# Performance work log

Measured on AMD Instinct MI355X. Metric: run time of the kernel, lower is better.

Reference implementation:

```python
import jax, jax.numpy as jnp
import numpy as np

LN_EPS = 1e-5

def setup_inputs() -> dict:
    key = jax.random.key(0)
    k1, k2, k3, k4 = jax.random.split(key, 4)
    B, N, D, E = 2, 50000, 128, 800000
    H = jax.random.normal(k1, (B, N, D), dtype=jnp.float32)
    src = jax.random.randint(k2, (E,), 0, N, dtype=jnp.int64)
    dst = jax.random.randint(k3, (E,), 0, N, dtype=jnp.int64)
    W = jax.random.normal(k4, (D, D), dtype=jnp.float32) * (1.0 / np.sqrt(D))
    gamma = jnp.ones((D,), dtype=jnp.float32)
    beta = jnp.zeros((D,), dtype=jnp.float32)
    return {"H": H, "src": src, "dst": dst, "W": W, "gamma": gamma, "beta": beta}

def reference(H, src, dst, W, gamma, beta):
    # m = Linear(H) (no bias): [B,N,D]
    m = jnp.einsum('bnd,de->bne', H, W)
    # gather messages at src, scatter-add into dst along node dim
    agg = jnp.zeros_like(m).at[:, dst, :].add(m[:, src, :])
    x = H + jax.nn.gelu(agg, approximate=False)
    # LayerNorm over last dim
    mu = jnp.mean(x, axis=-1, keepdims=True)
    var = jnp.var(x, axis=-1, keepdims=True)
    return (x - mu) * jax.lax.rsqrt(var + LN_EPS) * gamma + beta
```

## Files before the change

kernel.cpp:

```cpp
#include <hip/hip_runtime.h>
#include <math.h>

#define DIM 128
#define LN_EPS 1e-5f
#define CAP 64
#define TPW 2

typedef unsigned short bf16_t;
typedef unsigned short u16;
typedef __attribute__((ext_vector_type(8))) short bf16x8;
typedef __attribute__((ext_vector_type(4))) float f32x4;
typedef __attribute__((ext_vector_type(2))) float f32x2;

__device__ __forceinline__ bf16_t f2bf(float f) {
    unsigned u = __builtin_bit_cast(unsigned, f);
    u += 0x7FFFu + ((u >> 16) & 1u);
    return (bf16_t)(u >> 16);
}
__device__ __forceinline__ float lo_bf(unsigned u) {
    return __builtin_bit_cast(float, u << 16);
}
__device__ __forceinline__ float hi_bf(unsigned u) {
    return __builtin_bit_cast(float, u & 0xFFFF0000u);
}

__global__ __launch_bounds__(256) void prep_kernel(
    const float* __restrict__ W, bf16_t* __restrict__ WT,
    int* __restrict__ cursor, int N)
{
    const int tid = blockIdx.x * 256 + threadIdx.x;
    if (tid < N) cursor[tid] = 0;
    if (tid < (DIM * DIM / 4)) {
        const float4 w = ((const float4*)W)[tid];
        const int k  = tid >> 5;
        const int n0 = (tid & 31) * 4;
        WT[(n0 + 0) * DIM + k] = f2bf(w.x);
        WT[(n0 + 1) * DIM + k] = f2bf(w.y);
        WT[(n0 + 2) * DIM + k] = f2bf(w.z);
        WT[(n0 + 3) * DIM + k] = f2bf(w.w);
    }
}

__global__ __launch_bounds__(256, 2) void gemm_fill_kernel(
    const float* __restrict__ Hmat, const bf16_t* __restrict__ WT,
    bf16_t* __restrict__ Mout,
    const int* __restrict__ src, const int* __restrict__ dst,
    int* __restrict__ cursor, u16* __restrict__ eidxT,
    int nrows, int N, int E, int FB)
{
    if ((int)blockIdx.x < FB) {
        const int base = (blockIdx.x * 256 + threadIdx.x) * 8;
        if (base + 7 < E) {
            int4 da = *(const int4*)&dst[base];
            int4 db = *(const int4*)&dst[base + 4];
            int4 sa = *(const int4*)&src[base];
            int4 sb = *(const int4*)&src[base + 4];
            int p0 = atomicAdd(&cursor[da.x], 1);
            int p1 = atomicAdd(&cursor[da.y], 1);
            int p2 = atomicAdd(&cursor[da.z], 1);
            int p3 = atomicAdd(&cursor[da.w], 1);
            int p4 = atomicAdd(&cursor[db.x], 1);
            int p5 = atomicAdd(&cursor[db.y], 1);
            int p6 = atomicAdd(&cursor[db.z], 1);
            int p7 = atomicAdd(&cursor[db.w], 1);
            if (p0 < CAP) eidxT[(size_t)p0 * N + da.x] = (u16)sa.x;
            if (p1 < CAP) eidxT[(size_t)p1 * N + da.y] = (u16)sa.y;
            if (p2 < CAP) eidxT[(size_t)p2 * N + da.z] = (u16)sa.z;
            if (p3 < CAP) eidxT[(size_t)p3 * N + da.w] = (u16)sa.w;
            if (p4 < CAP) eidxT[(size_t)p4 * N + db.x] = (u16)sb.x;
            if (p5 < CAP) eidxT[(size_t)p5 * N + db.y] = (u16)sb.y;
            if (p6 < CAP) eidxT[(size_t)p6 * N + db.z] = (u16)sb.z;
            if (p7 < CAP) eidxT[(size_t)p7 * N + db.w] = (u16)sb.w;
        } else {
            for (int e = base; e < E; ++e) {
                int d = dst[e];
                int pos = atomicAdd(&cursor[d], 1);
                if (pos < CAP) eidxT[(size_t)pos * N + d] = (u16)src[e];
            }
        }
        return;
    }

    const int tid  = threadIdx.x;
    const int wave = tid >> 6;
    const int lane = tid & 63;
    const int quad = lane >> 4;
    const int l15  = lane & 15;

    bf16x8 wf[32];
    #pragma unroll
    for (int t = 0; t < 8; ++t)
        #pragma unroll
        for (int ks = 0; ks < 4; ++ks)
            wf[t * 4 + ks] = *(const bf16x8*)
                &WT[(size_t)(t * 16 + l15) * DIM + ks * 32 + quad * 8];

    const int gblock  = blockIdx.x - FB;
    const int baserow = (gblock * 4 + wave) * (TPW * 16);

    #pragma unroll
    for (int rt = 0; rt < TPW; ++rt) {
        const int arow = baserow + rt * 16 + l15;
        const float* Arow = Hmat + (size_t)((arow < nrows) ? arow : 0) * DIM;

        f32x4 acc[8];
        #pragma unroll
        for (int t = 0; t < 8; ++t) acc[t] = (f32x4){0.f, 0.f, 0.f, 0.f};

        #pragma unroll
        for (int ks = 0; ks < 4; ++ks) {
            const int k0 = ks * 32 + quad * 8;
            float4 a0 = *(const float4*)&Arow[k0];
            float4 a1 = *(const float4*)&Arow[k0 + 4];
            bf16x8 hf;
            hf[0] = (short)f2bf(a0.x); hf[1] = (short)f2bf(a0.y);
            hf[2] = (short)f2bf(a0.z); hf[3] = (short)f2bf(a0.w);
            hf[4] = (short)f2bf(a1.x); hf[5] = (short)f2bf(a1.y);
            hf[6] = (short)f2bf(a1.z); hf[7] = (short)f2bf(a1.w);

            #pragma unroll
            for (int t = 0; t < 8; ++t)
                acc[t] = __builtin_amdgcn_mfma_f32_16x16x32_bf16(
                             wf[t * 4 + ks], hf, acc[t], 0, 0, 0);
        }

        if (arow < nrows) {
            const int b = (arow >= N) ? 1 : 0;
            const int n = arow - (b ? N : 0);
            bf16_t* orow = Mout + ((size_t)n * 2 + b) * DIM;
            #pragma unroll
            for (int t = 0; t < 8; ++t) {
                ushort4 o;
                o.x = f2bf(acc[t][0]); o.y = f2bf(acc[t][1]);
                o.z = f2bf(acc[t][2]); o.w = f2bf(acc[t][3]);
                *(ushort4*)&orow[t * 16 + quad * 4] = o;
            }
        }
    }
}

__global__ __launch_bounds__(256) void gather_kernel(
    const bf16_t* __restrict__ M, const float* __restrict__ Hmat,
    const int* __restrict__ cursor, const u16* __restrict__ eidxT,
    const float* __restrict__ gamma, const float* __restrict__ beta,
    float* __restrict__ out, int N)
{
    const int wave = threadIdx.x >> 6;
    const int lane = threadIdx.x & 63;
    const int node = blockIdx.x * 4 + wave;
    if (node >= N) return;

    const int b  = lane >> 5;
    const int c4 = lane & 31;

    const size_t elembase = ((size_t)b * N + node) * DIM + c4 * 4;
    float4 h  = *(const float4*)&Hmat[elembase];
    float4 gm = *(const float4*)&gamma[c4 * 4];
    float4 bt = *(const float4*)&beta[c4 * 4];

    int cnt = cursor[node];
    if (cnt > CAP) cnt = CAP;

    int myidx = (lane < cnt) ? (int)eidxT[(size_t)lane * N + node] : 0;

    const uint2* M2 = (const uint2*)M;

    f32x2 accA = {0.f, 0.f}, accB = {0.f, 0.f};
    int j = 0;
    for (; j + 16 <= cnt; j += 16) {
        uint2 v[16];
        #pragma unroll
        for (int q = 0; q < 16; ++q) {
            int s = __builtin_amdgcn_readlane(myidx, j + q);
            v[q] = (M2 + ((size_t)s << 6))[lane];
        }
        #pragma unroll
        for (int q = 0; q < 16; ++q) {
            f32x2 p0 = { lo_bf(v[q].x), hi_bf(v[q].x) };
            f32x2 p1 = { lo_bf(v[q].y), hi_bf(v[q].y) };
            accA += p0;
            accB += p1;
        }
    }
    if (j < cnt) {
        uint2 v[16];
        #pragma unroll
        for (int q = 0; q < 16; ++q) {
            int s = __builtin_amdgcn_readlane(myidx, (j + q) & 63);
            v[q] = (M2 + ((size_t)s << 6))[lane];
        }
        #pragma unroll
        for (int q = 0; q < 16; ++q) {
            unsigned vx = (j + q < cnt) ? v[q].x : 0u;
            unsigned vy = (j + q < cnt) ? v[q].y : 0u;
            f32x2 p0 = { lo_bf(vx), hi_bf(vx) };
            f32x2 p1 = { lo_bf(vy), hi_bf(vy) };
            accA += p0;
            accB += p1;
        }
    }

    float acc0 = accA.x, acc1 = accA.y, acc2 = accB.x, acc3 = accB.y;

    const float inv_sqrt2 = 0.70710678118654752f;
    float x0 = h.x + 0.5f * acc0 * (1.f + erff(acc0 * inv_sqrt2));
    float x1 = h.y + 0.5f * acc1 * (1.f + erff(acc1 * inv_sqrt2));
    float x2 = h.z + 0.5f * acc2 * (1.f + erff(acc2 * inv_sqrt2));
    float x3 = h.w + 0.5f * acc3 * (1.f + erff(acc3 * inv_sqrt2));

    float s  = x0 + x1 + x2 + x3;
    float ss = x0 * x0 + x1 * x1 + x2 * x2 + x3 * x3;
    #pragma unroll
    for (int o = 16; o > 0; o >>= 1) {
        s  += __shfl_xor(s,  o, 64);
        ss += __shfl_xor(ss, o, 64);
    }
    const float mean = s * (1.f / DIM);
    const float var  = ss * (1.f / DIM) - mean * mean;
    const float inv  = rsqrtf(var + LN_EPS);

    float4 o;
    o.x = (x0 - mean) * inv * gm.x + bt.x;
    o.y = (x1 - mean) * inv * gm.y + bt.y;
    o.z = (x2 - mean) * inv * gm.z + bt.z;
    o.w = (x3 - mean) * inv * gm.w + bt.w;
    *(float4*)&out[elembase] = o;
}

extern "C" void kernel_launch(void* const* d_in, const int* in_sizes, int n_in,
                              void* d_out, int out_size, void* d_ws, size_t ws_size,
                              hipStream_t stream)
{
    const float* H     = (const float*)d_in[0];
    const int*   src   = (const int*)  d_in[1];
    const int*   dst   = (const int*)  d_in[2];
    const float* W     = (const float*)d_in[3];
    const float* gamma = (const float*)d_in[4];
    const float* beta  = (const float*)d_in[5];
    float* out = (float*)d_out;

    const int E     = in_sizes[1];
    const int total = in_sizes[0];
    const int nrows = total / DIM;
    const int N     = nrows / 2;

    char* ws = (char*)d_ws;
    bf16_t* Mbuf = (bf16_t*)ws;   ws += (size_t)total * sizeof(bf16_t);
    int* cursor  = (int*)ws;      ws += (size_t)N * sizeof(int);
    u16* eidxT   = (u16*)ws;      ws += (size_t)CAP * N * sizeof(u16);
    bf16_t* WT   = (bf16_t*)ws;   ws += (size_t)DIM * DIM * sizeof(bf16_t);

    const int prep_elems = (N > DIM * DIM / 4) ? N : DIM * DIM / 4;
    prep_kernel<<<(prep_elems + 255) / 256, 256, 0, stream>>>(W, WT, cursor, N);

    const int FB = (E + 2047) / 2048;
    const int ROWS_PER_BLOCK = 4 * TPW * 16;
    const int GB = (nrows + ROWS_PER_BLOCK - 1) / ROWS_PER_BLOCK;
    gemm_fill_kernel<<<FB + GB, 256, 0, stream>>>(H, WT, Mbuf, src, dst,
                                                  cursor, eidxT, nrows, N, E, FB);

    gather_kernel<<<(N + 3) / 4, 256, 0, stream>>>(Mbuf, H, cursor, eidxT,
                                                   gamma, beta, out, N);
}
```

Measured before the change: 226.5 us.

## Fuse prep, GEMM/fill and gather into one cooperative persistent kernel

Replaces the three kernel launches with a single cooperative persistent kernel that uses grid-wide syncs between the prep, GEMM-plus-edge-bucketing, and gather/LayerNorm phases. The block count comes from the occupancy query, and 3/8 of the blocks do the edge fill while the rest do the GEMM. The edge index layout changes from transposed [slot][node] to node-major [node][slot], and the gather unrolls 32 loads with per-element predicates. The aim is to remove launch gaps and tail effects. In exchange, grid.sync costs and the fixed split may leave the fill or GEMM side underused, and persistent grid-stride loops may lose some memory parallelism.

New measurement: 569.8 us. +151.5%, slower.

```diff
diff --git a/kernel.cpp b/kernel.cpp
--- a/kernel.cpp
+++ b/kernel.cpp
@@ -1,10 +1,13 @@
 #include <hip/hip_runtime.h>
+#include <hip/hip_cooperative_groups.h>
 #include <math.h>
+
+namespace cg = cooperative_groups;
 
 #define DIM 128
 #define LN_EPS 1e-5f
 #define CAP 64
-#define TPW 2
+#define NTHR 256
 
 typedef unsigned short bf16_t;
 typedef unsigned short u16;
@@ -24,207 +27,183 @@
     return __builtin_bit_cast(float, u & 0xFFFF0000u);
 }
 
-__global__ __launch_bounds__(256) void prep_kernel(
-    const float* __restrict__ W, bf16_t* __restrict__ WT,
-    int* __restrict__ cursor, int N)
+__global__ __launch_bounds__(256, 2) void coop_kernel(
+    const float* __restrict__ Hmat, const int* __restrict__ src,
+    const int* __restrict__ dst, const float* __restrict__ W,
+    const float* __restrict__ gamma, const float* __restrict__ beta,
+    float* __restrict__ out, bf16_t* __restrict__ Mout,
+    int* __restrict__ cursor, u16* __restrict__ eidx,
+    bf16_t* __restrict__ WTg, int N, int nrows, int E)
 {
-    const int tid = blockIdx.x * 256 + threadIdx.x;
-    if (tid < N) cursor[tid] = 0;
-    if (tid < (DIM * DIM / 4)) {
-        const float4 w = ((const float4*)W)[tid];
-        const int k  = tid >> 5;
-        const int n0 = (tid & 31) * 4;
-        WT[(n0 + 0) * DIM + k] = f2bf(w.x);
-        WT[(n0 + 1) * DIM + k] = f2bf(w.y);
-        WT[(n0 + 2) * DIM + k] = f2bf(w.z);
-        WT[(n0 + 3) * DIM + k] = f2bf(w.w);
+    cg::grid_group grid = cg::this_grid();
+    const int tid   = threadIdx.x;
+    const int nblk  = gridDim.x;
+    const int gtid  = blockIdx.x * NTHR + tid;
+    const int lane  = tid & 63;
+    const int wave  = tid >> 6;
+    const int quad  = lane >> 4;
+    const int l15   = lane & 15;
+
+    for (int i = gtid; i < N; i += nblk * NTHR) cursor[i] = 0;
+    if (gtid < DIM * DIM / 4) {
+        const float4 w = ((const float4*)W)[gtid];
+        const int k  = gtid >> 5;
+        const int n0 = (gtid & 31) * 4;
+        WTg[(n0 + 0) * DIM + k] = f2bf(w.x);
+        WTg[(n0 + 1) * DIM + k] = f2bf(w.y);
+        WTg[(n0 + 2) * DIM + k] = f2bf(w.z);
+        WTg[(n0 + 3) * DIM + k] = f2bf(w.w);
     }
-}
-
-__global__ __launch_bounds__(256, 2) void gemm_fill_kernel(
-    const float* __restrict__ Hmat, const bf16_t* __restrict__ WT,
-    bf16_t* __restrict__ Mout,
-    const int* __restrict__ src, const int* __restrict__ dst,
-    int* __restrict__ cursor, u16* __restrict__ eidxT,
-    int nrows, int N, int E, int FB)
-{
-    if ((int)blockIdx.x < FB) {
-        const int base = (blockIdx.x * 256 + threadIdx.x) * 8;
-        if (base + 7 < E) {
-            int4 da = *(const int4*)&dst[base];
-            int4 db = *(const int4*)&dst[base + 4];
-            int4 sa = *(const int4*)&src[base];
-            int4 sb = *(const int4*)&src[base + 4];
-            int p0 = atomicAdd(&cursor[da.x], 1);
-            int p1 = atomicAdd(&cursor[da.y], 1);
-            int p2 = atomicAdd(&cursor[da.z], 1);
-            int p3 = atomicAdd(&cursor[da.w], 1);
-            int p4 = atomicAdd(&cursor[db.x], 1);
-            int p5 = atomicAdd(&cursor[db.y], 1);
-            int p6 = atomicAdd(&cursor[db.z], 1);
-            int p7 = atomicAdd(&cursor[db.w], 1);
-            if (p0 < CAP) eidxT[(size_t)p0 * N + da.x] = (u16)sa.x;
-            if (p1 < CAP) eidxT[(size_t)p1 * N + da.y] = (u16)sa.y;
-            if (p2 < CAP) eidxT[(size_t)p2 * N + da.z] = (u16)sa.z;
-            if (p3 < CAP) eidxT[(size_t)p3 * N + da.w] = (u16)sa.w;
-            if (p4 < CAP) eidxT[(size_t)p4 * N + db.x] = (u16)sb.x;
-            if (p5 < CAP) eidxT[(size_t)p5 * N + db.y] = (u16)sb.y;
-            if (p6 < CAP) eidxT[(size_t)p6 * N + db.z] = (u16)sb.z;
-            if (p7 < CAP) eidxT[(size_t)p7 * N + db.w] = (u16)sb.w;
-        } else {
-            for (int e = base; e < E; ++e) {
-                int d = dst[e];
-                int pos = atomicAdd(&cursor[d], 1);
-                if (pos < CAP) eidxT[(size_t)pos * N + d] = (u16)src[e];
-            }
-        }
-        return;
+    __threadfence();
+    grid.sync();
+
+    const int FBLK = (nblk * 3) / 8;
+    if ((int)blockIdx.x < FBLK) {
+        const int nt = FBLK * NTHR;
+        for (int base = (blockIdx.x * NTHR + tid) * 8; base < E; base += nt * 8) {
+            if (base + 7 < E) {
+                int4 da = *(const int4*)&dst[base];
+                int4 db = *(const int4*)&dst[base + 4];
+                int4 sa = *(const int4*)&src[base];
+                int4 sb = *(const int4*)&src[base + 4];
+                int p0 = atomicAdd(&cursor[da.x], 1);
+                int p1 = atomicAdd(&cursor[da.y], 1);
+                int p2 = atomicAdd(&cursor[da.z], 1);
+                int p3 = atomicAdd(&cursor[da.w], 1);
+                int p4 = atomicAdd(&cursor[db.x], 1);
+                int p5 = atomicAdd(&cursor[db.y], 1);
+                int p6 = atomicAdd(&cursor[db.z], 1);
+                int p7 = atomicAdd(&cursor[db.w], 1);
+                if (p0 < CAP) eidx[(size_t)da.x * CAP + p0] = (u16)sa.x;
+                if (p1 < CAP) eidx[(size_t)da.y * CAP + p1] = (u16)sa.y;
+                if (p2 < CAP) eidx[(size_t)da.z * CAP + p2] = (u16)sa.z;
+                if (p3 < CAP) eidx[(size_t)da.w * CAP + p3] = (u16)sa.w;
+                if (p4 < CAP) eidx[(size_t)db.x * CAP + p4] = (u16)sb.x;
+                if (p5 < CAP) eidx[(size_t)db.y * CAP + p5] = (u16)sb.y;
+                if (p6 < CAP) eidx[(size_t)db.z * CAP + p6] = (u16)sb.z;
+                if (p7 < CAP) eidx[(size_t)db.w * CAP + p7] = (u16)sb.w;
+            } else {
+                for (int e = base; e < E; ++e) {
+                    int d = dst[e];
+                    int pos = atomicAdd(&cursor[d], 1);
+                    if (pos < CAP) eidx[(size_t)d * CAP + pos] = (u16)src[e];
+                }
+            }
+        }
+    } else {
+        bf16x8 wf[32];
+        #pragma unroll
+        for (int t = 0; t < 8; ++t)
+            #pragma unroll
+            for (int ks = 0; ks < 4; ++ks)
+                wf[t * 4 + ks] = *(const bf16x8*)
+                    &WTg[(size_t)(t * 16 + l15) * DIM + ks * 32 + quad * 8];
+
+        const int ntiles = (nrows + 15) / 16;
+        const int gw     = (nblk - FBLK) * 4;
+        for (int tile = (blockIdx.x - FBLK) * 4 + wave; tile < ntiles; tile += gw) {
+            const int arow = tile * 16 + l15;
+            const float* Arow = Hmat + (size_t)((arow < nrows) ? arow : 0) * DIM;
+
+            f32x4 acc[8];
+            #pragma unroll
+            for (int t = 0; t < 8; ++t) acc[t] = (f32x4){0.f, 0.f, 0.f, 0.f};
+
+            #pragma unroll
+            for (int ks = 0; ks < 4; ++ks) {
+                const int k0 = ks * 32 + quad * 8;
+                float4 a0 = *(const float4*)&Arow[k0];
+                float4 a1 = *(const float4*)&Arow[k0 + 4];
+                bf16x8 hf;
+                hf[0] = (short)f2bf(a0.x); hf[1] = (short)f2bf(a0.y);
+                hf[2] = (short)f2bf(a0.z); hf[3] = (short)f2bf(a0.w);
+                hf[4] = (short)f2bf(a1.x); hf[5] = (short)f2bf(a1.y);
+                hf[6] = (short)f2bf(a1.z); hf[7] = (short)f2bf(a1.w);
+
+                #pragma unroll
+                for (int t = 0; t < 8; ++t)
+                    acc[t] = __builtin_amdgcn_mfma_f32_16x16x32_bf16(
+                                 wf[t * 4 + ks], hf, acc[t], 0, 0, 0);
+            }
+
+            if (arow < nrows) {
+                const int b = (arow >= N) ? 1 : 0;
+                const int n = arow - (b ? N : 0);
+                bf16_t* orow = Mout + ((size_t)n * 2 + b) * DIM;
+                #pragma unroll
+                for (int t = 0; t < 8; ++t) {
+                    ushort4 o;
+                    o.x = f2bf(acc[t][0]); o.y = f2bf(acc[t][1]);
+                    o.z = f2bf(acc[t][2]); o.w = f2bf(acc[t][3]);
+                    *(ushort4*)&orow[t * 16 + quad * 4] = o;
+                }
+            }
+        }
     }
-
-    const int tid  = threadIdx.x;
-    const int wave = tid >> 6;
-    const int lane = tid & 63;
-    const int quad = lane >> 4;
-    const int l15  = lane & 15;
-
-    bf16x8 wf[32];
-    #pragma unroll
-    for (int t = 0; t < 8; ++t)
-        #pragma unroll
-        for (int ks = 0; ks < 4; ++ks)
-            wf[t * 4 + ks] = *(const bf16x8*)
-                &WT[(size_t)(t * 16 + l15) * DIM + ks * 32 + quad * 8];
-
-    const int gblock  = blockIdx.x - FB;
-    const int baserow = (gblock * 4 + wave) * (TPW * 16);
-
-    #pragma unroll
-    for (int rt = 0; rt < TPW; ++rt) {
-        const int arow = baserow + rt * 16 + l15;
-        const float* Arow = Hmat + (size_t)((arow < nrows) ? arow : 0) * DIM;
-
-        f32x4 acc[8];
-        #pragma unroll
-        for (int t = 0; t < 8; ++t) acc[t] = (f32x4){0.f, 0.f, 0.f, 0.f};
-
-        #pragma unroll
-        for (int ks = 0; ks < 4; ++ks) {
-            const int k0 = ks * 32 + quad * 8;
-            float4 a0 = *(const float4*)&Arow[k0];
-            float4 a1 = *(const float4*)&Arow[k0 + 4];
-            bf16x8 hf;
-            hf[0] = (short)f2bf(a0.x); hf[1] = (short)f2bf(a0.y);
-            hf[2] = (short)f2bf(a0.z); hf[3] = (short)f2bf(a0.w);
-            hf[4] = (short)f2bf(a1.x); hf[5] = (short)f2bf(a1.y);
-            hf[6] = (short)f2bf(a1.z); hf[7] = (short)f2bf(a1.w);
-
-            #pragma unroll
-            for (int t = 0; t < 8; ++t)
-                acc[t] = __builtin_amdgcn_mfma_f32_16x16x32_bf16(
-                             wf[t * 4 + ks], hf, acc[t], 0, 0, 0);
-        }
-
-        if (arow < nrows) {
-            const int b = (arow >= N) ? 1 : 0;
-            const int n = arow - (b ? N : 0);
-            bf16_t* orow = Mout + ((size_t)n * 2 + b) * DIM;
-            #pragma unroll
-            for (int t = 0; t < 8; ++t) {
-                ushort4 o;
-                o.x = f2bf(acc[t][0]); o.y = f2bf(acc[t][1]);
-                o.z = f2bf(acc[t][2]); o.w = f2bf(acc[t][3]);
-                *(ushort4*)&orow[t * 16 + quad * 4] = o;
-            }
-        }
-    }
-}
-
-__global__ __launch_bounds__(256) void gather_kernel(
-    const bf16_t* __restrict__ M, const float* __restrict__ Hmat,
-    const int* __restrict__ cursor, const u16* __restrict__ eidxT,
-    const float* __restrict__ gamma, const float* __restrict__ beta,
-    float* __restrict__ out, int N)
-{
-    const int wave = threadIdx.x >> 6;
-    const int lane = threadIdx.x & 63;
-    const int node = blockIdx.x * 4 + wave;
-    if (node >= N) return;
+    __threadfence();
+    grid.sync();
 
     const int b  = lane >> 5;
     const int c4 = lane & 31;
-
-    const size_t elembase = ((size_t)b * N + node) * DIM + c4 * 4;
-    float4 h  = *(const float4*)&Hmat[elembase];
+    const int nwaves = nblk * 4;
+    const uint2* M2  = (const uint2*)Mout;
+
     float4 gm = *(const float4*)&gamma[c4 * 4];
     float4 bt = *(const float4*)&beta[c4 * 4];
 
-    int cnt = cursor[node];
-    if (cnt > CAP) cnt = CAP;
-
-    int myidx = (lane < cnt) ? (int)eidxT[(size_t)lane * N + node] : 0;
-
-    const uint2* M2 = (const uint2*)M;
-
-    f32x2 accA = {0.f, 0.f}, accB = {0.f, 0.f};
-    int j = 0;
-    for (; j + 16 <= cnt; j += 16) {
-        uint2 v[16];
+    for (int node = blockIdx.x * 4 + wave; node < N; node += nwaves) {
+        int cnt = cursor[node];
+        if (cnt > CAP) cnt = CAP;
+
+        int myidx = (lane < cnt) ? (int)eidx[(size_t)node * CAP + lane] : 0;
+
+        const size_t elembase = ((size_t)b * N + node) * DIM + c4 * 4;
+        float4 h = *(const float4*)&Hmat[elembase];
+
+        f32x2 accA = {0.f, 0.f}, accB = {0.f, 0.f};
+        for (int j = 0; j < cnt; j += 32) {
+            uint2 v[32];
+            #pragma unroll
+            for (int q = 0; q < 32; ++q) {
+                if (j + q < cnt) {
+                    int s = __builtin_amdgcn_readlane(myidx, j + q);
+                    v[q] = (M2 + ((size_t)s << 6))[lane];
+                }
+            }
+            #pragma unroll
+            for (int q = 0; q < 32; ++q) {
+                if (j + q < cnt) {
+                    accA += (f32x2){ lo_bf(v[q].x), hi_bf(v[q].x) };
+                    accB += (f32x2){ lo_bf(v[q].y), hi_bf(v[q].y) };
+                }
+            }
+        }
+        float acc0 = accA.x, acc1 = accA.y, acc2 = accB.x, acc3 = accB.y;
+
+        const float inv_sqrt2 = 0.70710678118654752f;
+        float x0 = h.x + 0.5f * acc0 * (1.f + erff(acc0 * inv_sqrt2));
+        float x1 = h.y + 0.5f * acc1 * (1.f + erff(acc1 * inv_sqrt2));
+        float x2 = h.z + 0.5f * acc2 * (1.f + erff(acc2 * inv_sqrt2));
+        float x3 = h.w + 0.5f * acc3 * (1.f + erff(acc3 * inv_sqrt2));
+
+        float s  = x0 + x1 + x2 + x3;
+        float ss = x0 * x0 + x1 * x1 + x2 * x2 + x3 * x3;
         #pragma unroll
-        for (int q = 0; q < 16; ++q) {
-            int s = __builtin_amdgcn_readlane(myidx, j + q);
-            v[q] = (M2 + ((size_t)s << 6))[lane];
-        }
-        #pragma unroll
-        for (int q = 0; q < 16; ++q) {
-            f32x2 p0 = { lo_bf(v[q].x), hi_bf(v[q].x) };
-            f32x2 p1 = { lo_bf(v[q].y), hi_bf(v[q].y) };
-            accA += p0;
-            accB += p1;
-        }
+        for (int o = 16; o > 0; o >>= 1) {
+            s  += __shfl_xor(s,  o, 64);
+            ss += __shfl_xor(ss, o, 64);
+        }
+        const float mean = s * (1.f / DIM);
+        const float var  = ss * (1.f / DIM) - mean * mean;
+        const float inv  = rsqrtf(var + LN_EPS);
+
+        float4 o;
+        o.x = (x0 - mean) * inv * gm.x + bt.x;
+        o.y = (x1 - mean) * inv * gm.y + bt.y;
+        o.z = (x2 - mean) * inv * gm.z + bt.z;
+        o.w = (x3 - mean) * inv * gm.w + bt.w;
+        *(float4*)&out[elembase] = o;
     }
-    if (j < cnt) {
-        uint2 v[16];
-        #pragma unroll
-        for (int q = 0; q < 16; ++q) {
-            int s = __builtin_amdgcn_readlane(myidx, (j + q) & 63);
-            v[q] = (M2 + ((size_t)s << 6))[lane];
-        }
-        #pragma unroll
-        for (int q = 0; q < 16; ++q) {
-            unsigned vx = (j + q < cnt) ? v[q].x : 0u;
-            unsigned vy = (j + q < cnt) ? v[q].y : 0u;
-            f32x2 p0 = { lo_bf(vx), hi_bf(vx) };
-            f32x2 p1 = { lo_bf(vy), hi_bf(vy) };
-            accA += p0;
-            accB += p1;
-        }
-    }
-
-    float acc0 = accA.x, acc1 = accA.y, acc2 = accB.x, acc3 = accB.y;
-
-    const float inv_sqrt2 = 0.70710678118654752f;
-    float x0 = h.x + 0.5f * acc0 * (1.f + erff(acc0 * inv_sqrt2));
-    float x1 = h.y + 0.5f * acc1 * (1.f + erff(acc1 * inv_sqrt2));
-    float x2 = h.z + 0.5f * acc2 * (1.f + erff(acc2 * inv_sqrt2));
-    float x3 = h.w + 0.5f * acc3 * (1.f + erff(acc3 * inv_sqrt2));
-
-    float s  = x0 + x1 + x2 + x3;
-    float ss = x0 * x0 + x1 * x1 + x2 * x2 + x3 * x3;
-    #pragma unroll
-    for (int o = 16; o > 0; o >>= 1) {
-        s  += __shfl_xor(s,  o, 64);
-        ss += __shfl_xor(ss, o, 64);
-    }
-    const float mean = s * (1.f / DIM);
-    const float var  = ss * (1.f / DIM) - mean * mean;
-    const float inv  = rsqrtf(var + LN_EPS);
-
-    float4 o;
-    o.x = (x0 - mean) * inv * gm.x + bt.x;
-    o.y = (x1 - mean) * inv * gm.y + bt.y;
-    o.z = (x2 - mean) * inv * gm.z + bt.z;
-    o.w = (x3 - mean) * inv * gm.w + bt.w;
-    *(float4*)&out[elembase] = o;
 }
 
 extern "C" void kernel_launch(void* const* d_in, const int* in_sizes, int n_in,
@@ -239,26 +218,30 @@
     const float* beta  = (const float*)d_in[5];
     float* out = (float*)d_out;
 
-    const int E     = in_sizes[1];
-    const int total = in_sizes[0];
-    const int nrows = total / DIM;
-    const int N     = nrows / 2;
+    int E     = in_sizes[1];
+    int total = in_sizes[0];
+    int nrows = total / DIM;
+    int N     = nrows / 2;
 
     char* ws = (char*)d_ws;
     bf16_t* Mbuf = (bf16_t*)ws;   ws += (size_t)total * sizeof(bf16_t);
     int* cursor  = (int*)ws;      ws += (size_t)N * sizeof(int);
-    u16* eidxT   = (u16*)ws;      ws += (size_t)CAP * N * sizeof(u16);
+    u16* eidx    = (u16*)ws;      ws += (size_t)CAP * N * sizeof(u16);
     bf16_t* WT   = (bf16_t*)ws;   ws += (size_t)DIM * DIM * sizeof(bf16_t);
 
-    const int prep_elems = (N > DIM * DIM / 4) ? N : DIM * DIM / 4;
-    prep_kernel<<<(prep_elems + 255) / 256, 256, 0, stream>>>(W, WT, cursor, N);
-
-    const int FB = (E + 2047) / 2048;
-    const int ROWS_PER_BLOCK = 4 * TPW * 16;
-    const int GB = (nrows + ROWS_PER_BLOCK - 1) / ROWS_PER_BLOCK;
-    gemm_fill_kernel<<<FB + GB, 256, 0, stream>>>(H, WT, Mbuf, src, dst,
-                                                  cursor, eidxT, nrows, N, E, FB);
-
-    gather_kernel<<<(N + 3) / 4, 256, 0, stream>>>(Mbuf, H, cursor, eidxT,
-                                                   gamma, beta, out, N);
-}
+    int perCU = 0;
+    hipOccupancyMaxActiveBlocksPerMultiprocessor(&perCU, (const void*)coop_kernel,
+                                                 NTHR, 0);
+    if (perCU < 1) perCU = 1;
+    int nblk = perCU * 256;
+    if (nblk > 512) nblk = 512;
+
+    void* args[] = {
+        (void*)&H, (void*)&src, (void*)&dst, (void*)&W,
+        (void*)&gamma, (void*)&beta, (void*)&out, (void*)&Mbuf,
+        (void*)&cursor, (void*)&eidx, (void*)&WT,
+        (void*)&N, (void*)&nrows, (void*)&E
+    };
+    hipLaunchCooperativeKernel((const void*)coop_kernel, dim3(nblk), dim3(NTHR),
+                               args, 0, stream);
+}
```

## Replicate edge buckets per XCD with workgroup-scope atomics in fill

Applied to the files above, without the earlier changes.

The fill phase now keeps 8 copies of the per-node cursor and bucket, one per XCD. The XCD is read from the hardware register, and slots are claimed with relaxed workgroup-scope atomics, so cursor updates should stay within one XCD's L2 instead of going through device-wide coherence. Each bucket is now node-major with 16 slots per replica, so one wave can load a node's whole index list in a single coalesced read. The gather kernel walks the 8 replicas one after another and issues at most two row loads per step, which gives less memory-level parallelism than the earlier 16-deep batched loads. It also relies on workgroup-scope atomics being coherent across workgroups on the same XCD.

Result: no change. 230.6 us (+1.8%).

```diff
diff --git a/kernel.cpp b/kernel.cpp
--- a/kernel.cpp
+++ b/kernel.cpp
@@ -3,7 +3,8 @@
 
 #define DIM 128
 #define LN_EPS 1e-5f
-#define CAP 64
+#define NREP 8
+#define RCAP 16
 #define TPW 2
 
 typedef unsigned short bf16_t;
@@ -23,13 +24,18 @@
 __device__ __forceinline__ float hi_bf(unsigned u) {
     return __builtin_bit_cast(float, u & 0xFFFF0000u);
 }
+__device__ __forceinline__ int xcd_id() {
+    unsigned x;
+    asm volatile("s_getreg_b32 %0, hwreg(HW_REG_XCC_ID)" : "=s"(x));
+    return (int)(x & (NREP - 1));
+}
 
 __global__ __launch_bounds__(256) void prep_kernel(
     const float* __restrict__ W, bf16_t* __restrict__ WT,
     int* __restrict__ cursor, int N)
 {
     const int tid = blockIdx.x * 256 + threadIdx.x;
-    if (tid < N) cursor[tid] = 0;
+    if (tid < NREP * N) cursor[tid] = 0;
     if (tid < (DIM * DIM / 4)) {
         const float4 w = ((const float4*)W)[tid];
         const int k  = tid >> 5;
@@ -41,42 +47,42 @@
     }
 }
 
+__device__ __forceinline__ void bucket_push(
+    int* __restrict__ cursor, u16* __restrict__ eidx,
+    int node, int srcv, int xcc, int N)
+{
+    const size_t c = (size_t)xcc * N + node;
+    int pos = __hip_atomic_fetch_add(&cursor[c], 1,
+                                     __ATOMIC_RELAXED, __HIP_MEMORY_SCOPE_WORKGROUP);
+    if (pos < RCAP) eidx[c * RCAP + pos] = (u16)srcv;
+}
+
 __global__ __launch_bounds__(256, 2) void gemm_fill_kernel(
     const float* __restrict__ Hmat, const bf16_t* __restrict__ WT,
     bf16_t* __restrict__ Mout,
     const int* __restrict__ src, const int* __restrict__ dst,
-    int* __restrict__ cursor, u16* __restrict__ eidxT,
+    int* __restrict__ cursor, u16* __restrict__ eidx,
     int nrows, int N, int E, int FB)
 {
     if ((int)blockIdx.x < FB) {
+        const int xcc = xcd_id();
         const int base = (blockIdx.x * 256 + threadIdx.x) * 8;
         if (base + 7 < E) {
             int4 da = *(const int4*)&dst[base];
             int4 db = *(const int4*)&dst[base + 4];
             int4 sa = *(const int4*)&src[base];
             int4 sb = *(const int4*)&src[base + 4];
-            int p0 = atomicAdd(&cursor[da.x], 1);
-            int p1 = atomicAdd(&cursor[da.y], 1);
-            int p2 = atomicAdd(&cursor[da.z], 1);
-            int p3 = atomicAdd(&cursor[da.w], 1);
-            int p4 = atomicAdd(&cursor[db.x], 1);
-            int p5 = atomicAdd(&cursor[db.y], 1);
-            int p6 = atomicAdd(&cursor[db.z], 1);
-            int p7 = atomicAdd(&cursor[db.w], 1);
-            if (p0 < CAP) eidxT[(size_t)p0 * N + da.x] = (u16)sa.x;
-            if (p1 < CAP) eidxT[(size_t)p1 * N + da.y] = (u16)sa.y;
-            if (p2 < CAP) eidxT[(size_t)p2 * N + da.z] = (u16)sa.z;
-            if (p3 < CAP) eidxT[(size_t)p3 * N + da.w] = (u16)sa.w;
-            if (p4 < CAP) eidxT[(size_t)p4 * N + db.x] = (u16)sb.x;
-            if (p5 < CAP) eidxT[(size_t)p5 * N + db.y] = (u16)sb.y;
-            if (p6 < CAP) eidxT[(size_t)p6 * N + db.z] = (u16)sb.z;
-            if (p7 < CAP) eidxT[(size_t)p7 * N + db.w] = (u16)sb.w;
+            bucket_push(cursor, eidx, da.x, sa.x, xcc, N);
+            bucket_push(cursor, eidx, da.y, sa.y, xcc, N);
+            bucket_push(cursor, eidx, da.z, sa.z, xcc, N);
+            bucket_push(cursor, eidx, da.w, sa.w, xcc, N);
+            bucket_push(cursor, eidx, db.x, sb.x, xcc, N);
+            bucket_push(cursor, eidx, db.y, sb.y, xcc, N);
+            bucket_push(cursor, eidx, db.z, sb.z, xcc, N);
+            bucket_push(cursor, eidx, db.w, sb.w, xcc, N);
         } else {
-            for (int e = base; e < E; ++e) {
-                int d = dst[e];
-                int pos = atomicAdd(&cursor[d], 1);
-                if (pos < CAP) eidxT[(size_t)pos * N + d] = (u16)src[e];
-            }
+            for (int e = base; e < E; ++e)
+                bucket_push(cursor, eidx, dst[e], src[e], xcc, N);
         }
         return;
     }
@@ -141,7 +147,7 @@
 
 __global__ __launch_bounds__(256) void gather_kernel(
     const bf16_t* __restrict__ M, const float* __restrict__ Hmat,
-    const int* __restrict__ cursor, const u16* __restrict__ eidxT,
+    const int* __restrict__ cursor, const u16* __restrict__ eidx,
     const float* __restrict__ gamma, const float* __restrict__ beta,
     float* __restrict__ out, int N)
 {
@@ -158,48 +164,33 @@
     float4 gm = *(const float4*)&gamma[c4 * 4];
     float4 bt = *(const float4*)&beta[c4 * 4];
 
-    int cnt = cursor[node];
-    if (cnt > CAP) cnt = CAP;
-
-    int myidx = (lane < cnt) ? (int)eidxT[(size_t)lane * N + node] : 0;
+    int cval = 0;
+    if (lane < 8) cval = cursor[(size_t)lane * N + node];
+
+    const unsigned* eidx32 = (const unsigned*)eidx;
+    unsigned w = eidx32[((size_t)(lane >> 3) * N + node) * (RCAP / 2) + (lane & 7)];
 
     const uint2* M2 = (const uint2*)M;
-
     f32x2 accA = {0.f, 0.f}, accB = {0.f, 0.f};
-    int j = 0;
-    for (; j + 16 <= cnt; j += 16) {
-        uint2 v[16];
-        #pragma unroll
-        for (int q = 0; q < 16; ++q) {
-            int s = __builtin_amdgcn_readlane(myidx, j + q);
-            v[q] = (M2 + ((size_t)s << 6))[lane];
-        }
-        #pragma unroll
-        for (int q = 0; q < 16; ++q) {
-            f32x2 p0 = { lo_bf(v[q].x), hi_bf(v[q].x) };
-            f32x2 p1 = { lo_bf(v[q].y), hi_bf(v[q].y) };
-            accA += p0;
-            accB += p1;
-        }
-    }
-    if (j < cnt) {
-        uint2 v[16];
-        #pragma unroll
-        for (int q = 0; q < 16; ++q) {
-            int s = __builtin_amdgcn_readlane(myidx, (j + q) & 63);
-            v[q] = (M2 + ((size_t)s << 6))[lane];
-        }
-        #pragma unroll
-        for (int q = 0; q < 16; ++q) {
-            unsigned vx = (j + q < cnt) ? v[q].x : 0u;
-            unsigned vy = (j + q < cnt) ? v[q].y : 0u;
-            f32x2 p0 = { lo_bf(vx), hi_bf(vx) };
-            f32x2 p1 = { lo_bf(vy), hi_bf(vy) };
-            accA += p0;
-            accB += p1;
-        }
-    }
-
+
+    #pragma unroll
+    for (int r = 0; r < NREP; ++r) {
+        int cnt = __builtin_amdgcn_readlane(cval, r);
+        if (cnt > RCAP) cnt = RCAP;
+        for (int p = 0; p < cnt; p += 2) {
+            unsigned u = __builtin_amdgcn_readlane(w, r * 8 + (p >> 1));
+            int s0 = (int)(u & 0xFFFFu);
+            uint2 v0 = (M2 + ((size_t)s0 << 6))[lane];
+            accA += (f32x2){ lo_bf(v0.x), hi_bf(v0.x) };
+            accB += (f32x2){ lo_bf(v0.y), hi_bf(v0.y) };
+            if (p + 1 < cnt) {
+                int s1 = (int)(u >> 16);
+                uint2 v1 = (M2 + ((size_t)s1 << 6))[lane];
+                accA += (f32x2){ lo_bf(v1.x), hi_bf(v1.x) };
+                accB += (f32x2){ lo_bf(v1.y), hi_bf(v1.y) };
+            }
+        }
+    }
     float acc0 = accA.x, acc1 = accA.y, acc2 = accB.x, acc3 = accB.y;
 
     const float inv_sqrt2 = 0.70710678118654752f;
@@ -246,19 +237,19 @@
 
     char* ws = (char*)d_ws;
     bf16_t* Mbuf = (bf16_t*)ws;   ws += (size_t)total * sizeof(bf16_t);
-    int* cursor  = (int*)ws;      ws += (size_t)N * sizeof(int);
-    u16* eidxT   = (u16*)ws;      ws += (size_t)CAP * N * sizeof(u16);
+    int* cursor  = (int*)ws;      ws += (size_t)NREP * N * sizeof(int);
+    u16* eidx    = (u16*)ws;      ws += (size_t)NREP * N * RCAP * sizeof(u16);
     bf16_t* WT   = (bf16_t*)ws;   ws += (size_t)DIM * DIM * sizeof(bf16_t);
 
-    const int prep_elems = (N > DIM * DIM / 4) ? N : DIM * DIM / 4;
+    const int prep_elems = NREP * N;
     prep_kernel<<<(prep_elems + 255) / 256, 256, 0, stream>>>(W, WT, cursor, N);
 
     const int FB = (E + 2047) / 2048;
     const int ROWS_PER_BLOCK = 4 * TPW * 16;
     const int GB = (nrows + ROWS_PER_BLOCK - 1) / ROWS_PER_BLOCK;
     gemm_fill_kernel<<<FB + GB, 256, 0, stream>>>(H, WT, Mbuf, src, dst,
-                                                  cursor, eidxT, nrows, N, E, FB);
-
-    gather_kernel<<<(N + 3) / 4, 256, 0, stream>>>(Mbuf, H, cursor, eidxT,
+                                                  cursor, eidx, nrows, N, E, FB);
+
+    gather_kernel<<<(N + 3) / 4, 256, 0, stream>>>(Mbuf, H, cursor, eidx,
                                                    gamma, beta, out, N);
 }
```

## Replace global atomic edge bucketing with LDS histogram, scan and scatter

Applied to the files above, without the earlier changes.

Edge bucketing no longer uses global atomicAdd on a per-node cursor. It now runs as a counting sort: per-block shared-memory histograms with four 8-bit counters packed per word, a column-wise prefix scan fused into the GEMM launch, and a scatter pass that uses shared-memory atomics to rank edges within each block. The edge index table changes from slot-major to node-major, so each gather wave reads its neighbour list contiguously. The gather kernel also gets tighter launch bounds and sched_barriers to keep loads batched ahead of the accumulation. The cost is two extra kernel launches, a scatter pass that no longer overlaps the GEMM, and low-parallelism 64-block passes whose 8-bit packed counts assume few edges per node per block.

Result: slower. 277.0 us (+22.3%).

```diff
diff --git a/kernel.cpp b/kernel.cpp
--- a/kernel.cpp
+++ b/kernel.cpp
@@ -5,6 +5,8 @@
 #define LN_EPS 1e-5f
 #define CAP 64
 #define TPW 2
+#define FBLK 64
+#define MAXB 16384
 
 typedef unsigned short bf16_t;
 typedef unsigned short u16;
@@ -25,11 +27,9 @@
 }
 
 __global__ __launch_bounds__(256) void prep_kernel(
-    const float* __restrict__ W, bf16_t* __restrict__ WT,
-    int* __restrict__ cursor, int N)
+    const float* __restrict__ W, bf16_t* __restrict__ WT)
 {
     const int tid = blockIdx.x * 256 + threadIdx.x;
-    if (tid < N) cursor[tid] = 0;
     if (tid < (DIM * DIM / 4)) {
         const float4 w = ((const float4*)W)[tid];
         const int k  = tid >> 5;
@@ -41,42 +41,57 @@
     }
 }
 
-__global__ __launch_bounds__(256, 2) void gemm_fill_kernel(
+__global__ __launch_bounds__(256) void hist_kernel(
+    const int* __restrict__ dst, unsigned* __restrict__ hist,
+    int bins4, int E, int EPB)
+{
+    __shared__ unsigned hb[MAXB];
+    const int b   = blockIdx.x;
+    const int tid = threadIdx.x;
+    const int e0  = b * EPB;
+    const int e1  = (e0 + EPB < E) ? (e0 + EPB) : E;
+
+    for (int bin0 = 0; bin0 < bins4; bin0 += MAXB) {
+        const int nb = (bins4 - bin0 < MAXB) ? (bins4 - bin0) : MAXB;
+        for (int i = tid; i < nb; i += 256) hb[i] = 0;
+        __syncthreads();
+        for (int e = e0 + tid; e < e1; e += 256) {
+            const int d   = dst[e];
+            const int bin = (d >> 2) - bin0;
+            if (bin >= 0 && bin < nb)
+                atomicAdd(&hb[bin], 1u << ((d & 3) * 8));
+        }
+        __syncthreads();
+        for (int i = tid; i < nb; i += 256)
+            hist[(size_t)b * bins4 + bin0 + i] = hb[i];
+        __syncthreads();
+    }
+}
+
+__global__ __launch_bounds__(256, 2) void scan_gemm_kernel(
     const float* __restrict__ Hmat, const bf16_t* __restrict__ WT,
     bf16_t* __restrict__ Mout,
-    const int* __restrict__ src, const int* __restrict__ dst,
-    int* __restrict__ cursor, u16* __restrict__ eidxT,
-    int nrows, int N, int E, int FB)
-{
-    if ((int)blockIdx.x < FB) {
-        const int base = (blockIdx.x * 256 + threadIdx.x) * 8;
-        if (base + 7 < E) {
-            int4 da = *(const int4*)&dst[base];
-            int4 db = *(const int4*)&dst[base + 4];
-            int4 sa = *(const int4*)&src[base];
-            int4 sb = *(const int4*)&src[base + 4];
-            int p0 = atomicAdd(&cursor[da.x], 1);
-            int p1 = atomicAdd(&cursor[da.y], 1);
-            int p2 = atomicAdd(&cursor[da.z], 1);
-            int p3 = atomicAdd(&cursor[da.w], 1);
-            int p4 = atomicAdd(&cursor[db.x], 1);
-            int p5 = atomicAdd(&cursor[db.y], 1);
-            int p6 = atomicAdd(&cursor[db.z], 1);
-            int p7 = atomicAdd(&cursor[db.w], 1);
-            if (p0 < CAP) eidxT[(size_t)p0 * N + da.x] = (u16)sa.x;
-            if (p1 < CAP) eidxT[(size_t)p1 * N + da.y] = (u16)sa.y;
-            if (p2 < CAP) eidxT[(size_t)p2 * N + da.z] = (u16)sa.z;
-            if (p3 < CAP) eidxT[(size_t)p3 * N + da.w] = (u16)sa.w;
-            if (p4 < CAP) eidxT[(size_t)p4 * N + db.x] = (u16)sb.x;
-            if (p5 < CAP) eidxT[(size_t)p5 * N + db.y] = (u16)sb.y;
-            if (p6 < CAP) eidxT[(size_t)p6 * N + db.z] = (u16)sb.z;
-            if (p7 < CAP) eidxT[(size_t)p7 * N + db.w] = (u16)sb.w;
-        } else {
-            for (int e = base; e < E; ++e) {
-                int d = dst[e];
-                int pos = atomicAdd(&cursor[d], 1);
-                if (pos < CAP) eidxT[(size_t)pos * N + d] = (u16)src[e];
+    const unsigned* __restrict__ hist, unsigned* __restrict__ offs,
+    int* __restrict__ cursor,
+    int bins4, int N, int nrows, int SB)
+{
+    if ((int)blockIdx.x < SB) {
+        const int bin = blockIdx.x * 256 + threadIdx.x;
+        if (bin < bins4) {
+            unsigned l0 = 0, l1 = 0, l2 = 0, l3 = 0;
+            for (int b = 0; b < FBLK; ++b) {
+                const unsigned c = hist[(size_t)b * bins4 + bin];
+                offs[(size_t)b * bins4 + bin] =
+                    (l0 & 0xFFu) | ((l1 & 0xFFu) << 8) |
+                    ((l2 & 0xFFu) << 16) | ((l3 & 0xFFu) << 24);
+                l0 += c & 0xFFu;         l1 += (c >> 8) & 0xFFu;
+                l2 += (c >> 16) & 0xFFu; l3 += (c >> 24) & 0xFFu;
             }
+            const int n = bin * 4;
+            if (n     < N) cursor[n]     = (int)l0;
+            if (n + 1 < N) cursor[n + 1] = (int)l1;
+            if (n + 2 < N) cursor[n + 2] = (int)l2;
+            if (n + 3 < N) cursor[n + 3] = (int)l3;
         }
         return;
     }
@@ -95,7 +110,7 @@
             wf[t * 4 + ks] = *(const bf16x8*)
                 &WT[(size_t)(t * 16 + l15) * DIM + ks * 32 + quad * 8];
 
-    const int gblock  = blockIdx.x - FB;
+    const int gblock  = blockIdx.x - SB;
     const int baserow = (gblock * 4 + wave) * (TPW * 16);
 
     #pragma unroll
@@ -139,9 +154,40 @@
     }
 }
 
-__global__ __launch_bounds__(256) void gather_kernel(
+__global__ __launch_bounds__(256) void scatter_kernel(
+    const int* __restrict__ src, const int* __restrict__ dst,
+    const unsigned* __restrict__ offs, u16* __restrict__ eidx,
+    int bins4, int E, int EPB)
+{
+    __shared__ unsigned hb[MAXB];
+    const int b   = blockIdx.x;
+    const int tid = threadIdx.x;
+    const int e0  = b * EPB;
+    const int e1  = (e0 + EPB < E) ? (e0 + EPB) : E;
+
+    for (int bin0 = 0; bin0 < bins4; bin0 += MAXB) {
+        const int nb = (bins4 - bin0 < MAXB) ? (bins4 - bin0) : MAXB;
+        for (int i = tid; i < nb; i += 256) hb[i] = 0;
+        __syncthreads();
+        for (int e = e0 + tid; e < e1; e += 256) {
+            const int d   = dst[e];
+            const int bin = (d >> 2) - bin0;
+            if (bin >= 0 && bin < nb) {
+                const int sh = (d & 3) * 8;
+                const unsigned old = atomicAdd(&hb[bin], 1u << sh);
+                const int rank = (int)((old >> sh) & 0xFFu);
+                const int base = (int)((offs[(size_t)b * bins4 + (d >> 2)] >> sh) & 0xFFu);
+                const int slot = base + rank;
+                if (slot < CAP) eidx[(size_t)d * CAP + slot] = (u16)src[e];
+            }
+        }
+        __syncthreads();
+    }
+}
+
+__global__ __launch_bounds__(256, 3) void gather_kernel(
     const bf16_t* __restrict__ M, const float* __restrict__ Hmat,
-    const int* __restrict__ cursor, const u16* __restrict__ eidxT,
+    const int* __restrict__ cursor, const u16* __restrict__ eidx,
     const float* __restrict__ gamma, const float* __restrict__ beta,
     float* __restrict__ out, int N)
 {
@@ -161,11 +207,11 @@
     int cnt = cursor[node];
     if (cnt > CAP) cnt = CAP;
 
-    int myidx = (lane < cnt) ? (int)eidxT[(size_t)lane * N + node] : 0;
+    int myidx = (lane < cnt) ? (int)eidx[(size_t)node * CAP + lane] : 0;
 
     const uint2* M2 = (const uint2*)M;
-
     f32x2 accA = {0.f, 0.f}, accB = {0.f, 0.f};
+
     int j = 0;
     for (; j + 16 <= cnt; j += 16) {
         uint2 v[16];
@@ -174,12 +220,11 @@
             int s = __builtin_amdgcn_readlane(myidx, j + q);
             v[q] = (M2 + ((size_t)s << 6))[lane];
         }
+        __builtin_amdgcn_sched_barrier(0);
         #pragma unroll
         for (int q = 0; q < 16; ++q) {
-            f32x2 p0 = { lo_bf(v[q].x), hi_bf(v[q].x) };
-            f32x2 p1 = { lo_bf(v[q].y), hi_bf(v[q].y) };
-            accA += p0;
-            accB += p1;
+            accA += (f32x2){ lo_bf(v[q].x), hi_bf(v[q].x) };
+            accB += (f32x2){ lo_bf(v[q].y), hi_bf(v[q].y) };
         }
     }
     if (j < cnt) {
@@ -189,17 +234,15 @@
             int s = __builtin_amdgcn_readlane(myidx, (j + q) & 63);
             v[q] = (M2 + ((size_t)s << 6))[lane];
         }
+        __builtin_amdgcn_sched_barrier(0);
         #pragma unroll
         for (int q = 0; q < 16; ++q) {
             unsigned vx = (j + q < cnt) ? v[q].x : 0u;
             unsigned vy = (j + q < cnt) ? v[q].y : 0u;
-            f32x2 p0 = { lo_bf(vx), hi_bf(vx) };
-            f32x2 p1 = { lo_bf(vy), hi_bf(vy) };
-            accA += p0;
-            accB += p1;
-        }
-    }
-
+            accA += (f32x2){ lo_bf(vx), hi_bf(vx) };
+            accB += (f32x2){ lo_bf(vy), hi_bf(vy) };
+        }
+    }
     float acc0 = accA.x, acc1 = accA.y, acc2 = accB.x, acc3 = accB.y;
 
     const float inv_sqrt2 = 0.70710678118654752f;
@@ -244,21 +287,29 @@
     const int nrows = total / DIM;
     const int N     = nrows / 2;
 
+    const int bins4 = (N + 3) / 4;
+    const int EPB   = (E + FBLK - 1) / FBLK;
+
     char* ws = (char*)d_ws;
-    bf16_t* Mbuf = (bf16_t*)ws;   ws += (size_t)total * sizeof(bf16_t);
-    int* cursor  = (int*)ws;      ws += (size_t)N * sizeof(int);
-    u16* eidxT   = (u16*)ws;      ws += (size_t)CAP * N * sizeof(u16);
-    bf16_t* WT   = (bf16_t*)ws;   ws += (size_t)DIM * DIM * sizeof(bf16_t);
-
-    const int prep_elems = (N > DIM * DIM / 4) ? N : DIM * DIM / 4;
-    prep_kernel<<<(prep_elems + 255) / 256, 256, 0, stream>>>(W, WT, cursor, N);
-
-    const int FB = (E + 2047) / 2048;
+    bf16_t* Mbuf    = (bf16_t*)ws;   ws += (size_t)total * sizeof(bf16_t);
+    int* cursor     = (int*)ws;      ws += (size_t)N * sizeof(int);
+    u16* eidx       = (u16*)ws;      ws += (size_t)N * CAP * sizeof(u16);
+    bf16_t* WT      = (bf16_t*)ws;   ws += (size_t)DIM * DIM * sizeof(bf16_t);
+    unsigned* hist  = (unsigned*)ws; ws += (size_t)FBLK * bins4 * sizeof(unsigned);
+    unsigned* offs  = (unsigned*)ws; ws += (size_t)FBLK * bins4 * sizeof(unsigned);
+
+    prep_kernel<<<(DIM * DIM / 4 + 255) / 256, 256, 0, stream>>>(W, WT);
+
+    hist_kernel<<<FBLK, 256, 0, stream>>>(dst, hist, bins4, E, EPB);
+
+    const int SB = (bins4 + 255) / 256;
     const int ROWS_PER_BLOCK = 4 * TPW * 16;
     const int GB = (nrows + ROWS_PER_BLOCK - 1) / ROWS_PER_BLOCK;
-    gemm_fill_kernel<<<FB + GB, 256, 0, stream>>>(H, WT, Mbuf, src, dst,
-                                                  cursor, eidxT, nrows, N, E, FB);
-
-    gather_kernel<<<(N + 3) / 4, 256, 0, stream>>>(Mbuf, H, cursor, eidxT,
+    scan_gemm_kernel<<<SB + GB, 256, 0, stream>>>(H, WT, Mbuf, hist, offs,
+                                                  cursor, bins4, N, nrows, SB);
+
+    scatter_kernel<<<FBLK, 256, 0, stream>>>(src, dst, offs, eidx, bins4, E, EPB);
+
+    gather_kernel<<<(N + 3) / 4, 256, 0, stream>>>(Mbuf, H, cursor, eidx,
                                                    gamma, beta, out, N);
 }
```
